# Performance work log

Hardware: AMD Instinct MI355X
Metric: run time of the kernel (lower is better)

Reference implementation:

```python
import jax, jax.numpy as jnp
import numpy as np

# ---- dims ----
N = 16380      # atoms
R = 819        # residues
APR = 20       # atoms per residue
K = 16         # k_neighbors
H = 64         # hidden_mult (channels)
HEADS = 8
DH = H // HEADS
L = 6          # hidden_layers
BINS = 100
MIN_D, MAX_D = 0.0, 10.0
E_DIM = 64     # embed_dim
FFN = 2 * H    # mlp_ratio = 2


def setup_inputs() -> dict:
    key = jax.random.key(0)
    ks = jax.random.split(key, 22)
    g = lambda k, shape, fan: jax.random.normal(k, shape, jnp.float32) / np.sqrt(fan)
    return {
        'coords': jax.random.uniform(ks[0], (N, 3), jnp.float32) * 70.0,
        'atom_ids': jax.random.randint(ks[1], (N,), 0, 64),
        'res_ids': jax.random.randint(ks[2], (N,), 0, 8),
        'elem_ids': jax.random.randint(ks[3], (N,), 0, 16),
        'residue_index': jnp.repeat(jnp.arange(R), APR),
        'emb_atom': jax.random.normal(ks[4], (64, 32), jnp.float32),
        'emb_res': jax.random.normal(ks[5], (8, 16), jnp.float32),
        'emb_elem': jax.random.normal(ks[6], (16, 16), jnp.float32),
        'Win': g(ks[7], (E_DIM, H), E_DIM),
        'Wq': g(ks[8], (L, H, H), H),
        'Wk': g(ks[9], (L, H, H), H),
        'Wv': g(ks[10], (L, H, H), H),
        'Wvec': g(ks[11], (L, H, H), H),
        'wdir': jax.random.normal(ks[12], (L, H), jnp.float32) * 0.1,
        'dist_bias': jax.random.normal(ks[13], (L, BINS, HEADS), jnp.float32) * 0.1,
        'Wo': g(ks[14], (L, H, H), H),
        'W1': g(ks[15], (L, H, FFN), H),
        'W2': g(ks[16], (L, FFN, H), FFN),
        'Wg': g(ks[17], (L, H, H), H),
        'Wout': g(ks[18], (H, 2), H),
        'bout': jnp.zeros((2,), jnp.float32),
    }


def _ln(x):
    m = jnp.mean(x, axis=-1, keepdims=True)
    v = jnp.mean((x - m) ** 2, axis=-1, keepdims=True)
    return (x - m) * jax.lax.rsqrt(v + 1e-5)


def reference(coords, atom_ids, res_ids, elem_ids, residue_index,
              emb_atom, emb_res, emb_elem, Win, Wq, Wk, Wv, Wvec, wdir,
              dist_bias, Wo, W1, W2, Wg, Wout, bout):
    n = coords.shape[0]
    # --- polymer embedding: concat atom/residue/element embeddings ---
    feat = jnp.concatenate(
        [emb_atom[atom_ids], emb_res[res_ids], emb_elem[elem_ids]], axis=-1)  # (N, E_DIM)
    # --- kNN graph via dense pairwise distances (avoid (N,N,3) intermediate) ---
    sq = jnp.sum(coords * coords, axis=-1)
    d2 = sq[:, None] + sq[None, :] - 2.0 * (coords @ coords.T)     # (N, N)
    idx = jnp.arange(n)
    d2 = d2.at[idx, idx].set(jnp.inf)
    _, nbr = jax.lax.top_k(-d2, K)                                  # (N, K) src per dst
    # --- edge geometry: relative vector, distance, bin ---
    dvec = coords[:, None, :] - coords[nbr]                         # (N, K, 3) dst - src
    d = jnp.sqrt(jnp.sum(dvec * dvec, axis=-1) + 1e-12)
    dirn = dvec / d[..., None]
    bins = jnp.clip(((d - MIN_D) / (MAX_D - MIN_D) * BINS).astype(jnp.int32), 0, BINS - 1)
    # --- lift to hidden repr: scalars from embedding, vectors start at zero ---
    s = feat @ Win                                                  # (N, H) l=0 features
    v = jnp.zeros((n, H, 3), s.dtype)                               # (N, H, 3) l=1 features
    for l in range(L):
        h = _ln(s)
        q = (h @ Wq[l]).reshape(n, HEADS, DH)
        kf = (h @ Wk[l]).reshape(n, HEADS, DH)
        vf = (h @ Wv[l]).reshape(n, HEADS, DH)
        kn, vn = kf[nbr], vf[nbr]                                   # (N, K, HEADS, DH)
        logits = jnp.einsum('nhd,nkhd->nkh', q, kn) / np.sqrt(DH) + dist_bias[l][bins]
        attn = jax.nn.softmax(logits, axis=1)                       # softmax over K nbrs
        msg = jnp.einsum('nkh,nkhd->nhd', attn, vn).reshape(n, H)
        # equivariant vector messages: mixed source vectors + edge direction term
        vvals = jnp.einsum('nhc,hg->ngc', v, Wvec[l])               # (N, H, 3)
        vmsg = vvals[nbr] + wdir[l][None, None, :, None] * dirn[:, :, None, :]
        attn_c = jnp.repeat(attn, DH, axis=-1)                      # (N, K, H)
        vagg = jnp.einsum('nkh,nkhc->nhc', attn_c, vmsg)
        s = s + msg @ Wo[l]
        v = v + vagg
        h2 = _ln(s)
        s = s + jax.nn.gelu(h2 @ W1[l]) @ W2[l]                     # scalar FFN
        v = v * jax.nn.sigmoid(h2 @ Wg[l])[..., None]               # gated vector update
    # --- out repr is l=0 only; residue mean-pool then linear head ---
    res_feat = jax.ops.segment_sum(s, residue_index, num_segments=R) / APR
    return res_feat @ Wout + bout                                   # (R, 2)
```

## Files before the change

kernel.cpp:

```cpp
#include <hip/hip_runtime.h>
#include <cfloat>

#define NN    16380
#define RR    819
#define APR   20
#define KNB   16
#define HID   64
#define LAYERS 6
#define BINS  100
#define N64   (NN*HID)

#define ATB   32
#define NBLK  512
#define LDA   68
#define LDU   132
#define CSIZE 4.375f

#define OFF_QA    0
#define OFF_KA    (1*N64)
#define OFF_FA    (2*N64)
#define OFF_QB    (3*N64)
#define OFF_KB    (4*N64)
#define OFF_FB    (5*N64)
#define OFF_VA    (6*N64)
#define OFF_VB    (9*N64)
#define OFF_S     (12*N64)
#define OFF_DIRNS (13*N64)
#define OFF_C4    (OFF_DIRNS + NN*48)
#define OFF_C4S   (OFF_C4 + NN*4)
#define OFF_RES   (OFF_C4S + NN*4)
#define OFF_NBRS  (OFF_RES + RR*64)
#define OFF_BINSS (OFF_NBRS + NN*16)
#define OFF_O2N   (OFF_BINSS + NN*16)
#define OFF_N2O   (OFF_O2N + NN)
#define OFF_CELL  (OFF_N2O + NN)
#define OFF_HIST  (OFF_CELL + NN)
#define OFF_CNT   (OFF_HIST + 4096)
#define OFF_BASE  (OFF_CNT + 4096)

typedef unsigned long long u64;
#define U64MAX 0xFFFFFFFFFFFFFFFFull

__device__ __forceinline__ float gelu_f(float x) {
    float x3 = x*x*x;
    float t = tanhf(0.7978845608028654f*(x + 0.044715f*x3));
    return 0.5f*x*(1.0f+t);
}
__device__ __forceinline__ float sigmoid_f(float x) {
    return 1.0f/(1.0f + expf(-x));
}
__device__ __forceinline__ int spread3(int x) {
    return (x&1) | ((x&2)<<2) | ((x&4)<<4) | ((x&8)<<6);
}
__device__ __forceinline__ unsigned sortable_u32(float f) {
    unsigned u = __float_as_uint(f);
    return u ^ ((u & 0x80000000u) ? 0xFFFFFFFFu : 0x80000000u);
}

__global__ void pad_cell_kernel(const float* __restrict__ coords, float4* __restrict__ c4,
                                int* __restrict__ cellid, int* __restrict__ hist,
                                float* __restrict__ resb, int n) {
    int i = blockIdx.x*256 + threadIdx.x;
    for (int j = i; j < RR*HID; j += 16384) resb[j] = 0.f;
    if (i >= n) return;
    float x = coords[3*i], y = coords[3*i+1], z = coords[3*i+2];
    float sq = __fadd_rn(__fadd_rn(__fmul_rn(x,x), __fmul_rn(y,y)), __fmul_rn(z,z));
    c4[i] = make_float4(x, y, z, sq);
    int cx = min(15, max(0, (int)(x * (16.0f/70.0f))));
    int cy = min(15, max(0, (int)(y * (16.0f/70.0f))));
    int cz = min(15, max(0, (int)(z * (16.0f/70.0f))));
    int m = spread3(cx) | (spread3(cy)<<1) | (spread3(cz)<<2);
    cellid[i] = m;
    atomicAdd(&hist[m], 1);
}
__global__ void scan_kernel(const int* __restrict__ hist, int* __restrict__ base) {
    __shared__ int part[256];
    int t = threadIdx.x;
    int loc[16]; int s = 0;
    #pragma unroll
    for (int e = 0; e < 16; ++e) { loc[e] = s; s += hist[t*16+e]; }
    part[t] = s;
    __syncthreads();
    if (t == 0) { int acc = 0; for (int i = 0; i < 256; ++i) { int v = part[i]; part[i] = acc; acc += v; } }
    __syncthreads();
    int off = part[t];
    #pragma unroll
    for (int e = 0; e < 16; ++e) base[t*16+e] = off + loc[e];
}
__global__ void scatter_kernel(const int* __restrict__ cellid, const int* __restrict__ base,
                               int* __restrict__ cnt, int* __restrict__ o2n,
                               int* __restrict__ n2o, const float4* __restrict__ c4,
                               float4* __restrict__ c4s, int n) {
    int i = blockIdx.x*256 + threadIdx.x;
    if (i >= n) return;
    int m = cellid[i];
    int pos = base[m] + atomicAdd(&cnt[m], 1);
    o2n[i] = pos; n2o[pos] = i;
    c4s[pos] = c4[i];
}

#define SCRATCH 1024
__global__ __launch_bounds__(256) void knn_grid_kernel(
    const float4* __restrict__ c4s, const int* __restrict__ base, const int* __restrict__ hist,
    const int* __restrict__ n2o, const int* __restrict__ o2n,
    int* __restrict__ nbr, int* __restrict__ binsO, float* __restrict__ dirn, int n)
{
    __shared__ int sIdx[4][SCRATCH];
    int tid = threadIdx.x;
    int wv = tid >> 6, lane = tid & 63;
    int i = blockIdx.x*4 + wv;
    bool valid = i < n;
    int ii = valid ? i : 0;
    float4 cd = c4s[ii];
    float sqd = cd.w;
    int cx = min(15, max(0, (int)(cd.x * (16.0f/70.0f))));
    int cy = min(15, max(0, (int)(cd.y * (16.0f/70.0f))));
    int cz = min(15, max(0, (int)(cd.z * (16.0f/70.0f))));
    u64 dlist = U64MAX;
    u64 vmax  = U64MAX;
    int* sidx = sIdx[wv];

    auto compute_pk = [&](int idx) -> u64 {
        if (idx == i) return U64MAX;
        float4 cc = c4s[idx];
        float dt = __fmul_rn(cd.x, cc.x);
        dt = __fmaf_rn(cd.y, cc.y, dt);
        dt = __fmaf_rn(cd.z, cc.z, dt);
        float key = __fsub_rn(__fadd_rn(sqd, cc.w), __fmul_rn(2.0f, dt));
        int org = n2o[idx];
        return ((u64)sortable_u32(key) << 32) | (unsigned)org;
    };

    auto process_batch = [&](int M) {
        if (M <= 0) return;
        u64 lmin = U64MAX;
        for (int p = lane; p < M; p += 64) {
            u64 pk = compute_pk(sidx[p]);
            lmin = (pk < lmin) ? pk : lmin;
        }
        u64 T = lmin;
        #pragma unroll
        for (int off = 1; off < 64; off <<= 1) {
            u64 o = __shfl_xor(T, off);
            T = (o > T) ? o : T;
        }
        for (int c0 = 0; c0 < M; c0 += 64) {
            int p = c0 + lane;
            u64 mypk = (p < M) ? compute_pk(sidx[p]) : U64MAX;
            u64 bound = (vmax < T) ? vmax : T;
            unsigned long long mask = __ballot(mypk <= bound);
            while (mask) {
                int lb = (int)__builtin_ctzll(mask);
                mask &= mask - 1;
                u64 dc = __shfl(mypk, lb);
                if (dc < vmax) {
                    u64 dp = __shfl_up(dlist, 1);
                    bool below = dc < dlist;
                    bool take  = below && (lane == 0 || dc >= dp);
                    if (lane < 16) dlist = below ? (take ? dc : dp) : dlist;
                    vmax = __shfl(dlist, 15);
                }
            }
        }
    };

    for (int R = 1; R <= 16; ++R) {
        int side = 2*R+1;
        int ncell = side*side*side;
        int M = 0;
        for (int t0 = 0; t0 < ncell; t0 += 64) {
            int t = t0 + lane;
            int cnt = 0, b = 0;
            if (t < ncell) {
                int dxc = t % side - R;
                int dyc = (t/side) % side - R;
                int dzc = t/(side*side) - R;
                int ch = max(abs(dxc), max(abs(dyc), abs(dzc)));
                bool use = (R == 1) || (ch == R);
                int x = cx+dxc, y = cy+dyc, z = cz+dzc;
                if (use && x>=0 && x<16 && y>=0 && y<16 && z>=0 && z<16) {
                    int m = spread3(x) | (spread3(y)<<1) | (spread3(z)<<2);
                    cnt = hist[m]; b = base[m];
                }
            }
            int incl = cnt;
            #pragma unroll
            for (int o = 1; o < 64; o <<= 1) { int v = __shfl_up(incl, o); if (lane >= o) incl += v; }
            int excl = incl - cnt;
            int tot = __shfl(incl, 63);
            if (M + tot > SCRATCH) { process_batch(M); M = 0; }
            for (int e = 0; e < cnt; ++e) {
                int pos = M + excl + e;
                if (pos < SCRATCH) sidx[pos] = b + e;
            }
            M = min(M + tot, SCRATCH);
        }
        process_batch(M);
        float rim = (float)R * CSIZE;
        unsigned thS = sortable_u32(rim*rim - 0.05f);
        if ((unsigned)(vmax >> 32) < thS) break;
    }
    if (valid && lane < 16) {
        int org = (int)(dlist & 0xFFFFFFFFull);
        int src = o2n[org];
        float4 cs = c4s[src];
        float dx = __fsub_rn(cd.x, cs.x);
        float dy = __fsub_rn(cd.y, cs.y);
        float dz = __fsub_rn(cd.z, cs.z);
        float ss = __fadd_rn(__fadd_rn(__fmul_rn(dx,dx), __fmul_rn(dy,dy)),
                             __fmul_rn(dz,dz));
        float dd = __fsqrt_rn(__fadd_rn(ss, 1e-12f));
        nbr[i*KNB + lane] = src;
        float bf = __fmul_rn(__fdiv_rn(dd, 10.0f), 100.0f);
        int b = (int)bf;
        b = min(max(b, 0), BINS-1);
        binsO[i*KNB + lane] = b;
        dirn[i*48 + lane*3 + 0] = __fdiv_rn(dx, dd);
        dirn[i*48 + lane*3 + 1] = __fdiv_rn(dy, dd);
        dirn[i*48 + lane*3 + 2] = __fdiv_rn(dz, dd);
    }
}

__global__ __launch_bounds__(256) void prologue_kernel(
    const int* __restrict__ aid, const int* __restrict__ rid, const int* __restrict__ eid,
    const int* __restrict__ n2o,
    const float* __restrict__ ea, const float* __restrict__ er, const float* __restrict__ ee,
    const float* __restrict__ Win, const float* __restrict__ Wq, const float* __restrict__ Wk,
    const float* __restrict__ Wv,
    float* __restrict__ sg, float* __restrict__ qout, float* __restrict__ kout,
    float* __restrict__ vfout)
{
    __shared__ __align__(16) float sS[ATB*LDA];
    __shared__ __align__(16) float sH[ATB*LDA];
    __shared__ __align__(16) float sW[4096];
    const int tid = threadIdx.x;
    const int a0 = blockIdx.x*ATB;
    const int gi = tid>>4, gj = tid&15;
    const int lrow = tid>>3, lsub = tid&7;

    auto stageW = [&](const float* W) {
        const float4* src = (const float4*)W; float4* dst = (float4*)sW;
        #pragma unroll
        for (int r = 0; r < 4; ++r) dst[tid + 256*r] = src[tid + 256*r];
    };
    auto do_gemm = [&](const float* sA, float4& c0, float4& c1) {
        const float* a0p = sA + gi*LDA;
        const float* a1p = sA + (gi+16)*LDA;
        const float* wr  = sW + gj*4;
        #pragma unroll 8
        for (int k = 0; k < 64; ++k) {
            float av0 = a0p[k], av1 = a1p[k];
            float4 w = *(const float4*)(wr + k*64);
            c0.x = fmaf(av0,w.x,c0.x); c0.y = fmaf(av0,w.y,c0.y);
            c0.z = fmaf(av0,w.z,c0.z); c0.w = fmaf(av0,w.w,c0.w);
            c1.x = fmaf(av1,w.x,c1.x); c1.y = fmaf(av1,w.y,c1.y);
            c1.z = fmaf(av1,w.z,c1.z); c1.w = fmaf(av1,w.w,c1.w);
        }
    };
    auto do_ln = [&](const float* src, float* dst) {
        const float* sp = src + lrow*LDA + lsub*8;
        float v[8]; float s1 = 0.f;
        #pragma unroll
        for (int e = 0; e < 8; ++e) { v[e] = sp[e]; s1 += v[e]; }
        s1 += __shfl_xor(s1,1); s1 += __shfl_xor(s1,2); s1 += __shfl_xor(s1,4);
        float mean = s1*(1.0f/64.0f);
        float s2 = 0.f;
        #pragma unroll
        for (int e = 0; e < 8; ++e) { float t = v[e]-mean; s2 += t*t; }
        s2 += __shfl_xor(s2,1); s2 += __shfl_xor(s2,2); s2 += __shfl_xor(s2,4);
        float sc = 1.0f/sqrtf(s2*(1.0f/64.0f)+1e-5f);
        float* dp = dst + lrow*LDA + lsub*8;
        #pragma unroll
        for (int e = 0; e < 8; ++e) dp[e] = (v[e]-mean)*sc;
    };
    auto store_g = [&](float* base, float4 c0, float4 c1) {
        int g0 = a0+gi, g1 = a0+gi+16;
        if (g0 < NN) *(float4*)(base + (size_t)g0*64 + gj*4) = c0;
        if (g1 < NN) *(float4*)(base + (size_t)g1*64 + gj*4) = c1;
    };

    {
        int ga = a0 + lrow;
        int io = (ga < NN) ? n2o[ga] : 0;
        #pragma unroll
        for (int e = 0; e < 8; ++e) {
            int c = lsub*8 + e;
            float x = 0.f;
            if (ga < NN) {
                if (c < 32)      x = ea[aid[io]*32 + c];
                else if (c < 48) x = er[rid[io]*16 + (c-32)];
                else             x = ee[eid[io]*16 + (c-48)];
            }
            sH[lrow*LDA + c] = x;
        }
    }
    stageW(Win);
    __syncthreads();
    {
        float4 c0 = make_float4(0,0,0,0), c1 = c0;
        do_gemm(sH, c0, c1);
        *(float4*)(sS + gi*LDA + gj*4)      = c0;
        *(float4*)(sS + (gi+16)*LDA + gj*4) = c1;
        store_g(sg, c0, c1);
    }
    __syncthreads();
    do_ln(sS, sH);
    stageW(Wk);
    __syncthreads();
    { float4 c0 = make_float4(0,0,0,0), c1 = c0; do_gemm(sH, c0, c1); store_g(kout, c0, c1); }
    __syncthreads();
    stageW(Wv); __syncthreads();
    { float4 c0 = make_float4(0,0,0,0), c1 = c0; do_gemm(sH, c0, c1); store_g(vfout, c0, c1); }
    __syncthreads();
    stageW(Wq); __syncthreads();
    { float4 c0 = make_float4(0,0,0,0), c1 = c0; do_gemm(sH, c0, c1); store_g(qout, c0, c1); }
}

__global__ __launch_bounds__(256) void layer_kernel(
    const float* __restrict__ qin, const float* __restrict__ kin, const float* __restrict__ vfin,
    float* __restrict__ qout, float* __restrict__ kout, float* __restrict__ vfout,
    const float* __restrict__ vin, float* __restrict__ vout,
    float* __restrict__ sg, const float* __restrict__ dirn,
    const int* __restrict__ nbr, const int* __restrict__ bins,
    float* __restrict__ resb, const int* __restrict__ ridx, const int* __restrict__ n2o,
    const float* __restrict__ Wvec, const float* __restrict__ wdir,
    const float* __restrict__ dist_bias,
    const float* __restrict__ Wo, const float* __restrict__ W1, const float* __restrict__ W2,
    const float* __restrict__ Wg, const float* __restrict__ Wq, const float* __restrict__ Wk,
    const float* __restrict__ Wv, int l)
{
    __shared__ __align__(16) float sS[ATB*LDA];
    __shared__ __align__(16) float sH[ATB*LDA];
    __shared__ __align__(16) float sM[ATB*LDU];
    __shared__ __align__(16) float sVA[3][ATB*LDA];
    __shared__ __align__(16) float sW[4096];
    __shared__ float sDS[ATB*24];

    const int tid = threadIdx.x;
    const int bswz = (blockIdx.x & 7) * (NBLK/8) + (blockIdx.x >> 3);
    const int a0 = bswz*ATB;
    const int gi = tid>>4, gj = tid&15;
    const int lrow = tid>>3, lsub = tid&7;
    const int wv = tid>>6, lane = tid&63;

    const float* Wo_l = Wo + l*4096;
    const float* Wg_l = Wg + l*4096;
    const float* Wc_l = Wvec + l*4096;
    const float* W1_l = W1 + l*8192;
    const float* W2_l = W2 + l*8192;
    const float* db_l = dist_bias + l*BINS*8;
    const float* wd_l = wdir + l*64;

    auto stageW = [&](const float* W) {
        const float4* src = (const float4*)W; float4* dst = (float4*)sW;
        #pragma unroll
        for (int r = 0; r < 4; ++r) dst[tid + 256*r] = src[tid + 256*r];
    };
    auto stageW1h = [&](const float* W1l, int h) {
        const float4* src = (const float4*)W1l; float4* dst = (float4*)sW;
        #pragma unroll
        for (int r = 0; r < 4; ++r) {
            int q = tid + 256*r;
            int row = q >> 4, c4i = q & 15;
            dst[q] = src[row*32 + h*16 + c4i];
        }
    };
    auto do_gemm = [&](const float* sA, int lda, int ko, float4& c0, float4& c1) {
        const float* a0p = sA + gi*lda + ko;
        const float* a1p = sA + (gi+16)*lda + ko;
        const float* wr  = sW + gj*4;
        #pragma unroll 8
        for (int k = 0; k < 64; ++k) {
            float av0 = a0p[k], av1 = a1p[k];
            float4 w = *(const float4*)(wr + k*64);
            c0.x = fmaf(av0,w.x,c0.x); c0.y = fmaf(av0,w.y,c0.y);
            c0.z = fmaf(av0,w.z,c0.z); c0.w = fmaf(av0,w.w,c0.w);
            c1.x = fmaf(av1,w.x,c1.x); c1.y = fmaf(av1,w.y,c1.y);
            c1.z = fmaf(av1,w.z,c1.z); c1.w = fmaf(av1,w.w,c1.w);
        }
    };
    auto do_ln = [&](const float* src, float* dst) {
        const float* sp = src + lrow*LDA + lsub*8;
        float v[8]; float s1 = 0.f;
        #pragma unroll
        for (int e = 0; e < 8; ++e) { v[e] = sp[e]; s1 += v[e]; }
        s1 += __shfl_xor(s1,1); s1 += __shfl_xor(s1,2); s1 += __shfl_xor(s1,4);
        float mean = s1*(1.0f/64.0f);
        float s2 = 0.f;
        #pragma unroll
        for (int e = 0; e < 8; ++e) { float t = v[e]-mean; s2 += t*t; }
        s2 += __shfl_xor(s2,1); s2 += __shfl_xor(s2,2); s2 += __shfl_xor(s2,4);
        float sc = 1.0f/sqrtf(s2*(1.0f/64.0f)+1e-5f);
        float* dp = dst + lrow*LDA + lsub*8;
        #pragma unroll
        for (int e = 0; e < 8; ++e) dp[e] = (v[e]-mean)*sc;
    };
    auto store_g = [&](float* base, float4 c0, float4 c1) {
        int g0 = a0+gi, g1 = a0+gi+16;
        if (g0 < NN) *(float4*)(base + (size_t)g0*64 + gj*4) = c0;
        if (g1 < NN) *(float4*)(base + (size_t)g1*64 + gj*4) = c1;
    };

    {
        int ga = a0 + lrow;
        float4 z = make_float4(0,0,0,0);
        float4 x0 = z, x1 = z;
        if (ga < NN) {
            const float4* sp = (const float4*)(sg + (size_t)ga*64);
            x0 = sp[lsub*2]; x1 = sp[lsub*2+1];
        }
        float4* dp = (float4*)(sS + lrow*LDA);
        dp[lsub*2] = x0; dp[lsub*2+1] = x1;
    }
    stageW(Wo_l);

    for (int aa = 0; aa < 8; ++aa) {
        int la = wv*8 + aa;
        int ga = a0 + la;
        if (ga >= NN) break;
        float qh = qin[(size_t)ga*64 + lane];
        float lg[KNB]; int nb[KNB];
        #pragma unroll
        for (int k = 0; k < KNB; ++k) {
            int j = nbr[ga*KNB + k];
            nb[k] = j;
            float t = qh * kin[(size_t)j*64 + lane];
            t += __shfl_xor(t,1); t += __shfl_xor(t,2); t += __shfl_xor(t,4);
            lg[k] = t*0.35355339059327373f + db_l[bins[ga*KNB+k]*8 + (lane>>3)];
        }
        float m = lg[0];
        #pragma unroll
        for (int k = 1; k < KNB; ++k) m = fmaxf(m, lg[k]);
        float ssum = 0.f;
        #pragma unroll
        for (int k = 0; k < KNB; ++k) { lg[k] = expf(lg[k]-m); ssum += lg[k]; }
        float inv = 1.0f/ssum;
        float mh=0.f, b0=0.f, b1=0.f, b2=0.f, s0=0.f, s1=0.f, s2=0.f;
        if (l > 0) {
            #pragma unroll
            for (int k = 0; k < KNB; ++k) {
                float w = lg[k]*inv; int j = nb[k];
                mh += w * vfin[(size_t)j*64 + lane];
                b0 += w * vin[(size_t)j*64 + lane];
                b1 += w * vin[(size_t)N64 + (size_t)j*64 + lane];
                b2 += w * vin[2*(size_t)N64 + (size_t)j*64 + lane];
                s0 += w * dirn[ga*48 + k*3 + 0];
                s1 += w * dirn[ga*48 + k*3 + 1];
                s2 += w * dirn[ga*48 + k*3 + 2];
            }
            sVA[0][la*LDA + lane] = b0;
            sVA[1][la*LDA + lane] = b1;
            sVA[2][la*LDA + lane] = b2;
        } else {
            #pragma unroll
            for (int k = 0; k < KNB; ++k) {
                float w = lg[k]*inv; int j = nb[k];
                mh += w * vfin[(size_t)j*64 + lane];
                s0 += w * dirn[ga*48 + k*3 + 0];
                s1 += w * dirn[ga*48 + k*3 + 1];
                s2 += w * dirn[ga*48 + k*3 + 2];
            }
        }
        sM[la*LDU + lane] = mh;
        if ((lane & 7) == 0) {
            int hh = lane >> 3;
            sDS[la*24 + 0*8 + hh] = s0;
            sDS[la*24 + 1*8 + hh] = s1;
            sDS[la*24 + 2*8 + hh] = s2;
        }
    }
    __syncthreads();

    {
        float4 c0 = *(float4*)(sS + gi*LDA + gj*4);
        float4 c1 = *(float4*)(sS + (gi+16)*LDA + gj*4);
        do_gemm(sM, LDU, 0, c0, c1);
        *(float4*)(sS + gi*LDA + gj*4)      = c0;
        *(float4*)(sS + (gi+16)*LDA + gj*4) = c1;
    }
    __syncthreads();

    do_ln(sS, sH);
    stageW(Wg_l);
    __syncthreads();

    {
        float4 g0 = make_float4(0,0,0,0), g1 = g0;
        do_gemm(sH, LDA, 0, g0, g1);
        g0.x=sigmoid_f(g0.x); g0.y=sigmoid_f(g0.y); g0.z=sigmoid_f(g0.z); g0.w=sigmoid_f(g0.w);
        g1.x=sigmoid_f(g1.x); g1.y=sigmoid_f(g1.y); g1.z=sigmoid_f(g1.z); g1.w=sigmoid_f(g1.w);
        __syncthreads();
        stageW(Wc_l); __syncthreads();
        float4 wd4 = *(const float4*)&wd_l[gj*4];
        int g0i = a0+gi, g1i = a0+gi+16;
        #pragma unroll
        for (int p = 0; p < 3; ++p) {
            float4 t0 = make_float4(0,0,0,0), t1 = t0;
            if (l > 0) do_gemm(sVA[p], LDA, 0, t0, t1);
            float sp0 = sDS[gi*24 + p*8 + (gj>>1)];
            float sp1 = sDS[(gi+16)*24 + p*8 + (gj>>1)];
            if (g0i < NN) {
                float4 vi = make_float4(0,0,0,0);
                if (l > 0) vi = *(const float4*)(vin + (size_t)p*N64 + (size_t)g0i*64 + gj*4);
                float4 o;
                o.x = (vi.x + t0.x + wd4.x*sp0)*g0.x;
                o.y = (vi.y + t0.y + wd4.y*sp0)*g0.y;
                o.z = (vi.z + t0.z + wd4.z*sp0)*g0.z;
                o.w = (vi.w + t0.w + wd4.w*sp0)*g0.w;
                *(float4*)(vout + (size_t)p*N64 + (size_t)g0i*64 + gj*4) = o;
            }
            if (g1i < NN) {
                float4 vi = make_float4(0,0,0,0);
                if (l > 0) vi = *(const float4*)(vin + (size_t)p*N64 + (size_t)g1i*64 + gj*4);
                float4 o;
                o.x = (vi.x + t1.x + wd4.x*sp1)*g1.x;
                o.y = (vi.y + t1.y + wd4.y*sp1)*g1.y;
                o.z = (vi.z + t1.z + wd4.z*sp1)*g1.z;
                o.w = (vi.w + t1.w + wd4.w*sp1)*g1.w;
                *(float4*)(vout + (size_t)p*N64 + (size_t)g1i*64 + gj*4) = o;
            }
        }
    }
    __syncthreads();

    stageW1h(W1_l, 0); __syncthreads();
    float4 u0a, u1a;
    {
        float4 c0 = make_float4(0,0,0,0), c1 = c0;
        do_gemm(sH, LDA, 0, c0, c1);
        c0.x=gelu_f(c0.x); c0.y=gelu_f(c0.y); c0.z=gelu_f(c0.z); c0.w=gelu_f(c0.w);
        c1.x=gelu_f(c1.x); c1.y=gelu_f(c1.y); c1.z=gelu_f(c1.z); c1.w=gelu_f(c1.w);
        u0a = c0; u1a = c1;
    }
    __syncthreads();
    *(float4*)(sM + gi*LDU + gj*4)      = u0a;
    *(float4*)(sM + (gi+16)*LDU + gj*4) = u1a;
    stageW1h(W1_l, 1);
    __syncthreads();
    float4 u0b, u1b;
    {
        float4 c0 = make_float4(0,0,0,0), c1 = c0;
        do_gemm(sH, LDA, 0, c0, c1);
        c0.x=gelu_f(c0.x); c0.y=gelu_f(c0.y); c0.z=gelu_f(c0.z); c0.w=gelu_f(c0.w);
        c1.x=gelu_f(c1.x); c1.y=gelu_f(c1.y); c1.z=gelu_f(c1.z); c1.w=gelu_f(c1.w);
        u0b = c0; u1b = c1;
    }
    __syncthreads();
    *(float4*)(sM + gi*LDU + 64 + gj*4)      = u0b;
    *(float4*)(sM + (gi+16)*LDU + 64 + gj*4) = u1b;
    stageW(W2_l);
    __syncthreads();
    {
        float4 c0 = *(float4*)(sS + gi*LDA + gj*4);
        float4 c1 = *(float4*)(sS + (gi+16)*LDA + gj*4);
        do_gemm(sM, LDU, 0, c0, c1);
        __syncthreads();
        stageW(W2_l + 4096); __syncthreads();
        do_gemm(sM, LDU, 64, c0, c1);
        *(float4*)(sS + gi*LDA + gj*4)      = c0;
        *(float4*)(sS + (gi+16)*LDA + gj*4) = c1;
    }
    __syncthreads();

    if (l < LAYERS-1) {
        do_ln(sS, sH);
        stageW(Wk + (l+1)*4096);
        __syncthreads();
        { float4 c0 = make_float4(0,0,0,0), c1 = c0; do_gemm(sH, LDA, 0, c0, c1); store_g(kout, c0, c1); }
        __syncthreads();
        stageW(Wv + (l+1)*4096); __syncthreads();
        { float4 c0 = make_float4(0,0,0,0), c1 = c0; do_gemm(sH, LDA, 0, c0, c1); store_g(vfout, c0, c1); }
        __syncthreads();
        stageW(Wq + (l+1)*4096); __syncthreads();
        { float4 c0 = make_float4(0,0,0,0), c1 = c0; do_gemm(sH, LDA, 0, c0, c1); store_g(qout, c0, c1); }
        {
            int ga = a0 + lrow;
            if (ga < NN) {
                float4* dp = (float4*)(sg + (size_t)ga*64);
                const float4* sp = (const float4*)(sS + lrow*LDA);
                dp[lsub*2] = sp[lsub*2]; dp[lsub*2+1] = sp[lsub*2+1];
            }
        }
    } else {
        int ga = a0 + lrow;
        if (ga < NN) {
            int r = ridx[n2o[ga]];
            #pragma unroll
            for (int e = 0; e < 8; ++e)
                atomicAdd(&resb[r*64 + lsub*8 + e], sS[lrow*LDA + lsub*8 + e]);
        }
    }
}

__global__ void head_kernel(const float* __restrict__ res, const float* __restrict__ Wout,
                            const float* __restrict__ bout, float* __restrict__ out, int r_total) {
    int wave = threadIdx.x >> 6, lane = threadIdx.x & 63;
    int r = blockIdx.x*4 + wave;
    if (r >= r_total) return;
    float p = res[r*HID + lane] * (1.0f/APR);
    float o0 = p * Wout[lane*2 + 0];
    float o1 = p * Wout[lane*2 + 1];
    #pragma unroll
    for (int off = 1; off < 64; off <<= 1) { o0 += __shfl_xor(o0, off); o1 += __shfl_xor(o1, off); }
    if (lane == 0) { out[r*2+0] = o0 + bout[0]; out[r*2+1] = o1 + bout[1]; }
}

extern "C" void kernel_launch(void* const* d_in, const int* in_sizes, int n_in,
                              void* d_out, int out_size, void* d_ws, size_t ws_size,
                              hipStream_t stream) {
    const float* coords    = (const float*)d_in[0];
    const int*   atom_ids  = (const int*)d_in[1];
    const int*   res_ids   = (const int*)d_in[2];
    const int*   elem_ids  = (const int*)d_in[3];
    const int*   ridx      = (const int*)d_in[4];
    const float* emb_atom  = (const float*)d_in[5];
    const float* emb_res   = (const float*)d_in[6];
    const float* emb_elem  = (const float*)d_in[7];
    const float* Win       = (const float*)d_in[8];
    const float* Wq        = (const float*)d_in[9];
    const float* Wk        = (const float*)d_in[10];
    const float* Wv        = (const float*)d_in[11];
    const float* Wvec      = (const float*)d_in[12];
    const float* wdir      = (const float*)d_in[13];
    const float* dist_bias = (const float*)d_in[14];
    const float* Wo        = (const float*)d_in[15];
    const float* W1        = (const float*)d_in[16];
    const float* W2        = (const float*)d_in[17];
    const float* Wg        = (const float*)d_in[18];
    const float* Wout      = (const float*)d_in[19];
    const float* bout      = (const float*)d_in[20];
    float* out = (float*)d_out;

    float* ws = (float*)d_ws;
    float* qA = ws + OFF_QA;  float* kA = ws + OFF_KA;  float* fA = ws + OFF_FA;
    float* qB = ws + OFF_QB;  float* kB = ws + OFF_KB;  float* fB = ws + OFF_FB;
    float* vA = ws + OFF_VA;  float* vB = ws + OFF_VB;
    float* sg = ws + OFF_S;
    float* dirn_s = ws + OFF_DIRNS;
    float4* c4  = (float4*)(ws + OFF_C4);
    float4* c4s = (float4*)(ws + OFF_C4S);
    float* resb = ws + OFF_RES;
    int* nbr_s  = (int*)(ws + OFF_NBRS);
    int* bins_s = (int*)(ws + OFF_BINSS);
    int* o2n    = (int*)(ws + OFF_O2N);
    int* n2o    = (int*)(ws + OFF_N2O);
    int* cellid = (int*)(ws + OFF_CELL);
    int* hist   = (int*)(ws + OFF_HIST);
    int* cnt    = (int*)(ws + OFF_CNT);
    int* baseb  = (int*)(ws + OFF_BASE);

    hipMemsetAsync(hist, 0, 2*4096*sizeof(int), stream);

    pad_cell_kernel<<<(NN+255)/256, 256, 0, stream>>>(coords, c4, cellid, hist, resb, NN);
    scan_kernel<<<1, 256, 0, stream>>>(hist, baseb);
    scatter_kernel<<<(NN+255)/256, 256, 0, stream>>>(cellid, baseb, cnt, o2n, n2o, c4, c4s, NN);
    knn_grid_kernel<<<(NN+3)/4, 256, 0, stream>>>(c4s, baseb, hist, n2o, o2n, nbr_s, bins_s, dirn_s, NN);

    prologue_kernel<<<NBLK, 256, 0, stream>>>(atom_ids, res_ids, elem_ids, n2o,
                                              emb_atom, emb_res, emb_elem,
                                              Win, Wq, Wk, Wv, sg, qA, kA, fA);
    for (int l = 0; l < LAYERS; ++l) {
        int p = l & 1;
        const float* qin = p ? qB : qA;  float* qout = p ? qA : qB;
        const float* kin = p ? kB : kA;  float* kout = p ? kA : kB;
        const float* fin = p ? fB : fA;  float* fout = p ? fA : fB;
        const float* vin = p ? vB : vA;  float* vout = p ? vA : vB;
        layer_kernel<<<NBLK, 256, 0, stream>>>(qin, kin, fin, qout, kout, fout,
                                               vin, vout, sg, dirn_s, nbr_s, bins_s,
                                               resb, ridx, n2o,
                                               Wvec, wdir, dist_bias,
                                               Wo, W1, W2, Wg, Wq, Wk, Wv, l);
    }
    head_kernel<<<(RR+3)/4, 256, 0, stream>>>(resb, Wout, bout, out, RR);
}
```

Baseline: 604.4 us.

## Double layer_kernel threads to 512 and shrink shared memory per block

The layer kernel now launches 512 threads per 32-atom block. Each thread computes one float4 output row tile instead of two, and each wave handles 4 atoms instead of 8 in the attention gather. Vector aggregates are kept in registers and streamed through one shared tile per component, and the FFN hidden is processed in two 64-wide halves. These changes drop the large sM (LDU=132) and the sVA buffers, cutting LDS per block so more waves can be resident and gather latency is hidden better. In exchange there are extra barriers and staging passes, and each weight tile is reused across fewer outputs per thread.

```diff
diff --git a/kernel.cpp b/kernel.cpp
--- a/kernel.cpp
+++ b/kernel.cpp
@@ -13,7 +13,6 @@
 #define ATB   32
 #define NBLK  512
 #define LDA   68
-#define LDU   132
 #define CSIZE 4.375f
 
 #define OFF_QA    0
@@ -316,7 +315,7 @@
     { float4 c0 = make_float4(0,0,0,0), c1 = c0; do_gemm(sH, c0, c1); store_g(qout, c0, c1); }
 }
 
-__global__ __launch_bounds__(256) void layer_kernel(
+__global__ __launch_bounds__(512, 4) void layer_kernel(
     const float* __restrict__ qin, const float* __restrict__ kin, const float* __restrict__ vfin,
     float* __restrict__ qout, float* __restrict__ kout, float* __restrict__ vfout,
     const float* __restrict__ vin, float* __restrict__ vout,
@@ -331,8 +330,7 @@
 {
     __shared__ __align__(16) float sS[ATB*LDA];
     __shared__ __align__(16) float sH[ATB*LDA];
-    __shared__ __align__(16) float sM[ATB*LDU];
-    __shared__ __align__(16) float sVA[3][ATB*LDA];
+    __shared__ __align__(16) float sM[ATB*LDA];
     __shared__ __align__(16) float sW[4096];
     __shared__ float sDS[ATB*24];
 
@@ -340,7 +338,6 @@
     const int bswz = (blockIdx.x & 7) * (NBLK/8) + (blockIdx.x >> 3);
     const int a0 = bswz*ATB;
     const int gi = tid>>4, gj = tid&15;
-    const int lrow = tid>>3, lsub = tid&7;
     const int wv = tid>>6, lane = tid&63;
 
     const float* Wo_l = Wo + l*4096;
@@ -353,80 +350,75 @@
 
     auto stageW = [&](const float* W) {
         const float4* src = (const float4*)W; float4* dst = (float4*)sW;
-        #pragma unroll
-        for (int r = 0; r < 4; ++r) dst[tid + 256*r] = src[tid + 256*r];
+        dst[tid]       = src[tid];
+        dst[tid + 512] = src[tid + 512];
     };
     auto stageW1h = [&](const float* W1l, int h) {
         const float4* src = (const float4*)W1l; float4* dst = (float4*)sW;
         #pragma unroll
-        for (int r = 0; r < 4; ++r) {
-            int q = tid + 256*r;
+        for (int r = 0; r < 2; ++r) {
+            int q = tid + 512*r;
             int row = q >> 4, c4i = q & 15;
             dst[q] = src[row*32 + h*16 + c4i];
         }
     };
-    auto do_gemm = [&](const float* sA, int lda, int ko, float4& c0, float4& c1) {
-        const float* a0p = sA + gi*lda + ko;
-        const float* a1p = sA + (gi+16)*lda + ko;
-        const float* wr  = sW + gj*4;
+    auto do_gemm = [&](const float* sA, int lda, int ko, float4& c0) {
+        const float* ap = sA + gi*lda + ko;
+        const float* wr = sW + gj*4;
         #pragma unroll 8
         for (int k = 0; k < 64; ++k) {
-            float av0 = a0p[k], av1 = a1p[k];
+            float av = ap[k];
             float4 w = *(const float4*)(wr + k*64);
-            c0.x = fmaf(av0,w.x,c0.x); c0.y = fmaf(av0,w.y,c0.y);
-            c0.z = fmaf(av0,w.z,c0.z); c0.w = fmaf(av0,w.w,c0.w);
-            c1.x = fmaf(av1,w.x,c1.x); c1.y = fmaf(av1,w.y,c1.y);
-            c1.z = fmaf(av1,w.z,c1.z); c1.w = fmaf(av1,w.w,c1.w);
+            c0.x = fmaf(av,w.x,c0.x); c0.y = fmaf(av,w.y,c0.y);
+            c0.z = fmaf(av,w.z,c0.z); c0.w = fmaf(av,w.w,c0.w);
         }
     };
     auto do_ln = [&](const float* src, float* dst) {
-        const float* sp = src + lrow*LDA + lsub*8;
-        float v[8]; float s1 = 0.f;
-        #pragma unroll
-        for (int e = 0; e < 8; ++e) { v[e] = sp[e]; s1 += v[e]; }
-        s1 += __shfl_xor(s1,1); s1 += __shfl_xor(s1,2); s1 += __shfl_xor(s1,4);
+        const float* sp = src + gi*LDA + gj*4;
+        float v[4]; float s1 = 0.f;
+        #pragma unroll
+        for (int e = 0; e < 4; ++e) { v[e] = sp[e]; s1 += v[e]; }
+        s1 += __shfl_xor(s1,1); s1 += __shfl_xor(s1,2);
+        s1 += __shfl_xor(s1,4); s1 += __shfl_xor(s1,8);
         float mean = s1*(1.0f/64.0f);
         float s2 = 0.f;
         #pragma unroll
-        for (int e = 0; e < 8; ++e) { float t = v[e]-mean; s2 += t*t; }
-        s2 += __shfl_xor(s2,1); s2 += __shfl_xor(s2,2); s2 += __shfl_xor(s2,4);
+        for (int e = 0; e < 4; ++e) { float t = v[e]-mean; s2 += t*t; }
+        s2 += __shfl_xor(s2,1); s2 += __shfl_xor(s2,2);
+        s2 += __shfl_xor(s2,4); s2 += __shfl_xor(s2,8);
         float sc = 1.0f/sqrtf(s2*(1.0f/64.0f)+1e-5f);
-        float* dp = dst + lrow*LDA + lsub*8;
-        #pragma unroll
-        for (int e = 0; e < 8; ++e) dp[e] = (v[e]-mean)*sc;
-    };
-    auto store_g = [&](float* base, float4 c0, float4 c1) {
-        int g0 = a0+gi, g1 = a0+gi+16;
+        float* dp = dst + gi*LDA + gj*4;
+        #pragma unroll
+        for (int e = 0; e < 4; ++e) dp[e] = (v[e]-mean)*sc;
+    };
+    auto store_g = [&](float* base, float4 c0) {
+        int g0 = a0+gi;
         if (g0 < NN) *(float4*)(base + (size_t)g0*64 + gj*4) = c0;
-        if (g1 < NN) *(float4*)(base + (size_t)g1*64 + gj*4) = c1;
     };
 
     {
-        int ga = a0 + lrow;
-        float4 z = make_float4(0,0,0,0);
-        float4 x0 = z, x1 = z;
-        if (ga < NN) {
-            const float4* sp = (const float4*)(sg + (size_t)ga*64);
-            x0 = sp[lsub*2]; x1 = sp[lsub*2+1];
-        }
-        float4* dp = (float4*)(sS + lrow*LDA);
-        dp[lsub*2] = x0; dp[lsub*2+1] = x1;
+        int ga = a0 + gi;
+        float4 x = make_float4(0,0,0,0);
+        if (ga < NN) x = ((const float4*)(sg + (size_t)ga*64))[gj];
+        ((float4*)(sS + gi*LDA))[gj] = x;
     }
     stageW(Wo_l);
 
-    for (int aa = 0; aa < 8; ++aa) {
-        int la = wv*8 + aa;
+    float bx[4], by[4], bz[4];
+    #pragma unroll
+    for (int aa = 0; aa < 4; ++aa) {
+        int la = wv*4 + aa;
         int ga = a0 + la;
-        if (ga >= NN) break;
-        float qh = qin[(size_t)ga*64 + lane];
+        int gq = (ga < NN) ? ga : (NN-1);
+        float qh = qin[(size_t)gq*64 + lane];
         float lg[KNB]; int nb[KNB];
         #pragma unroll
         for (int k = 0; k < KNB; ++k) {
-            int j = nbr[ga*KNB + k];
+            int j = nbr[gq*KNB + k];
             nb[k] = j;
             float t = qh * kin[(size_t)j*64 + lane];
             t += __shfl_xor(t,1); t += __shfl_xor(t,2); t += __shfl_xor(t,4);
-            lg[k] = t*0.35355339059327373f + db_l[bins[ga*KNB+k]*8 + (lane>>3)];
+            lg[k] = t*0.35355339059327373f + db_l[bins[gq*KNB+k]*8 + (lane>>3)];
         }
         float m = lg[0];
         #pragma unroll
@@ -444,24 +436,22 @@
                 b0 += w * vin[(size_t)j*64 + lane];
                 b1 += w * vin[(size_t)N64 + (size_t)j*64 + lane];
                 b2 += w * vin[2*(size_t)N64 + (size_t)j*64 + lane];
-                s0 += w * dirn[ga*48 + k*3 + 0];
-                s1 += w * dirn[ga*48 + k*3 + 1];
-                s2 += w * dirn[ga*48 + k*3 + 2];
-            }
-            sVA[0][la*LDA + lane] = b0;
-            sVA[1][la*LDA + lane] = b1;
-            sVA[2][la*LDA + lane] = b2;
+                s0 += w * dirn[gq*48 + k*3 + 0];
+                s1 += w * dirn[gq*48 + k*3 + 1];
+                s2 += w * dirn[gq*48 + k*3 + 2];
+            }
         } else {
             #pragma unroll
             for (int k = 0; k < KNB; ++k) {
                 float w = lg[k]*inv; int j = nb[k];
                 mh += w * vfin[(size_t)j*64 + lane];
-                s0 += w * dirn[ga*48 + k*3 + 0];
-                s1 += w * dirn[ga*48 + k*3 + 1];
-                s2 += w * dirn[ga*48 + k*3 + 2];
-            }
-        }
-        sM[la*LDU + lane] = mh;
+                s0 += w * dirn[gq*48 + k*3 + 0];
+                s1 += w * dirn[gq*48 + k*3 + 1];
+                s2 += w * dirn[gq*48 + k*3 + 2];
+            }
+        }
+        bx[aa] = b0; by[aa] = b1; bz[aa] = b2;
+        sM[la*LDA + lane] = mh;
         if ((lane & 7) == 0) {
             int hh = lane >> 3;
             sDS[la*24 + 0*8 + hh] = s0;
@@ -472,11 +462,9 @@
     __syncthreads();
 
     {
-        float4 c0 = *(float4*)(sS + gi*LDA + gj*4);
-        float4 c1 = *(float4*)(sS + (gi+16)*LDA + gj*4);
-        do_gemm(sM, LDU, 0, c0, c1);
-        *(float4*)(sS + gi*LDA + gj*4)      = c0;
-        *(float4*)(sS + (gi+16)*LDA + gj*4) = c1;
+        float4 c0 = ((float4*)(sS + gi*LDA))[gj];
+        do_gemm(sM, LDA, 0, c0);
+        ((float4*)(sS + gi*LDA))[gj] = c0;
     }
     __syncthreads();
 
@@ -484,110 +472,106 @@
     stageW(Wg_l);
     __syncthreads();
 
+    float4 g0v = make_float4(0,0,0,0);
+    do_gemm(sH, LDA, 0, g0v);
+    g0v.x = sigmoid_f(g0v.x); g0v.y = sigmoid_f(g0v.y);
+    g0v.z = sigmoid_f(g0v.z); g0v.w = sigmoid_f(g0v.w);
+    __syncthreads();
+
+    float4 wd4 = *(const float4*)&wd_l[gj*4];
+    const int gidx = a0 + gi;
+    if (l > 0) {
+        stageW(Wc_l);
+        #pragma unroll
+        for (int p = 0; p < 3; ++p) {
+            #pragma unroll
+            for (int aa = 0; aa < 4; ++aa) {
+                int la = wv*4 + aa;
+                float bv = (p==0) ? bx[aa] : (p==1) ? by[aa] : bz[aa];
+                sM[la*LDA + lane] = bv;
+            }
+            __syncthreads();
+            float4 t0 = make_float4(0,0,0,0);
+            do_gemm(sM, LDA, 0, t0);
+            float sp0 = sDS[gi*24 + p*8 + (gj>>1)];
+            if (gidx < NN) {
+                float4 vi = *(const float4*)(vin + (size_t)p*N64 + (size_t)gidx*64 + gj*4);
+                float4 o;
+                o.x = (vi.x + t0.x + wd4.x*sp0)*g0v.x;
+                o.y = (vi.y + t0.y + wd4.y*sp0)*g0v.y;
+                o.z = (vi.z + t0.z + wd4.z*sp0)*g0v.z;
+                o.w = (vi.w + t0.w + wd4.w*sp0)*g0v.w;
+                *(float4*)(vout + (size_t)p*N64 + (size_t)gidx*64 + gj*4) = o;
+            }
+            __syncthreads();
+        }
+    } else {
+        #pragma unroll
+        for (int p = 0; p < 3; ++p) {
+            float sp0 = sDS[gi*24 + p*8 + (gj>>1)];
+            if (gidx < NN) {
+                float4 o;
+                o.x = (wd4.x*sp0)*g0v.x;
+                o.y = (wd4.y*sp0)*g0v.y;
+                o.z = (wd4.z*sp0)*g0v.z;
+                o.w = (wd4.w*sp0)*g0v.w;
+                *(float4*)(vout + (size_t)p*N64 + (size_t)gidx*64 + gj*4) = o;
+            }
+        }
+    }
+
+    stageW1h(W1_l, 0); __syncthreads();
+    float4 ua;
     {
-        float4 g0 = make_float4(0,0,0,0), g1 = g0;
-        do_gemm(sH, LDA, 0, g0, g1);
-        g0.x=sigmoid_f(g0.x); g0.y=sigmoid_f(g0.y); g0.z=sigmoid_f(g0.z); g0.w=sigmoid_f(g0.w);
-        g1.x=sigmoid_f(g1.x); g1.y=sigmoid_f(g1.y); g1.z=sigmoid_f(g1.z); g1.w=sigmoid_f(g1.w);
-        __syncthreads();
-        stageW(Wc_l); __syncthreads();
-        float4 wd4 = *(const float4*)&wd_l[gj*4];
-        int g0i = a0+gi, g1i = a0+gi+16;
-        #pragma unroll
-        for (int p = 0; p < 3; ++p) {
-            float4 t0 = make_float4(0,0,0,0), t1 = t0;
-            if (l > 0) do_gemm(sVA[p], LDA, 0, t0, t1);
-            float sp0 = sDS[gi*24 + p*8 + (gj>>1)];
-            float sp1 = sDS[(gi+16)*24 + p*8 + (gj>>1)];
-            if (g0i < NN) {
-                float4 vi = make_float4(0,0,0,0);
-                if (l > 0) vi = *(const float4*)(vin + (size_t)p*N64 + (size_t)g0i*64 + gj*4);
-                float4 o;
-                o.x = (vi.x + t0.x + wd4.x*sp0)*g0.x;
-                o.y = (vi.y + t0.y + wd4.y*sp0)*g0.y;
-                o.z = (vi.z + t0.z + wd4.z*sp0)*g0.z;
-                o.w = (vi.w + t0.w + wd4.w*sp0)*g0.w;
-                *(float4*)(vout + (size_t)p*N64 + (size_t)g0i*64 + gj*4) = o;
-            }
-            if (g1i < NN) {
-                float4 vi = make_float4(0,0,0,0);
-                if (l > 0) vi = *(const float4*)(vin + (size_t)p*N64 + (size_t)g1i*64 + gj*4);
-                float4 o;
-                o.x = (vi.x + t1.x + wd4.x*sp1)*g1.x;
-                o.y = (vi.y + t1.y + wd4.y*sp1)*g1.y;
-                o.z = (vi.z + t1.z + wd4.z*sp1)*g1.z;
-                o.w = (vi.w + t1.w + wd4.w*sp1)*g1.w;
-                *(float4*)(vout + (size_t)p*N64 + (size_t)g1i*64 + gj*4) = o;
-            }
-        }
-    }
-    __syncthreads();
-
-    stageW1h(W1_l, 0); __syncthreads();
-    float4 u0a, u1a;
+        float4 c = make_float4(0,0,0,0);
+        do_gemm(sH, LDA, 0, c);
+        ua.x = gelu_f(c.x); ua.y = gelu_f(c.y); ua.z = gelu_f(c.z); ua.w = gelu_f(c.w);
+    }
+    __syncthreads();
+    ((float4*)(sM + gi*LDA))[gj] = ua;
+    stageW(W2_l);
+    __syncthreads();
+    float4 acc = ((float4*)(sS + gi*LDA))[gj];
+    do_gemm(sM, LDA, 0, acc);
+    __syncthreads();
+    stageW1h(W1_l, 1); __syncthreads();
+    float4 ub;
     {
-        float4 c0 = make_float4(0,0,0,0), c1 = c0;
-        do_gemm(sH, LDA, 0, c0, c1);
-        c0.x=gelu_f(c0.x); c0.y=gelu_f(c0.y); c0.z=gelu_f(c0.z); c0.w=gelu_f(c0.w);
-        c1.x=gelu_f(c1.x); c1.y=gelu_f(c1.y); c1.z=gelu_f(c1.z); c1.w=gelu_f(c1.w);
-        u0a = c0; u1a = c1;
-    }
-    __syncthreads();
-    *(float4*)(sM + gi*LDU + gj*4)      = u0a;
-    *(float4*)(sM + (gi+16)*LDU + gj*4) = u1a;
-    stageW1h(W1_l, 1);
-    __syncthreads();
-    float4 u0b, u1b;
-    {
-        float4 c0 = make_float4(0,0,0,0), c1 = c0;
-        do_gemm(sH, LDA, 0, c0, c1);
-        c0.x=gelu_f(c0.x); c0.y=gelu_f(c0.y); c0.z=gelu_f(c0.z); c0.w=gelu_f(c0.w);
-        c1.x=gelu_f(c1.x); c1.y=gelu_f(c1.y); c1.z=gelu_f(c1.z); c1.w=gelu_f(c1.w);
-        u0b = c0; u1b = c1;
-    }
-    __syncthreads();
-    *(float4*)(sM + gi*LDU + 64 + gj*4)      = u0b;
-    *(float4*)(sM + (gi+16)*LDU + 64 + gj*4) = u1b;
-    stageW(W2_l);
-    __syncthreads();
-    {
-        float4 c0 = *(float4*)(sS + gi*LDA + gj*4);
-        float4 c1 = *(float4*)(sS + (gi+16)*LDA + gj*4);
-        do_gemm(sM, LDU, 0, c0, c1);
-        __syncthreads();
-        stageW(W2_l + 4096); __syncthreads();
-        do_gemm(sM, LDU, 64, c0, c1);
-        *(float4*)(sS + gi*LDA + gj*4)      = c0;
-        *(float4*)(sS + (gi+16)*LDA + gj*4) = c1;
-    }
+        float4 c = make_float4(0,0,0,0);
+        do_gemm(sH, LDA, 0, c);
+        ub.x = gelu_f(c.x); ub.y = gelu_f(c.y); ub.z = gelu_f(c.z); ub.w = gelu_f(c.w);
+    }
+    __syncthreads();
+    ((float4*)(sM + gi*LDA))[gj] = ub;
+    stageW(W2_l + 4096);
+    __syncthreads();
+    do_gemm(sM, LDA, 0, acc);
+    ((float4*)(sS + gi*LDA))[gj] = acc;
     __syncthreads();
 
     if (l < LAYERS-1) {
         do_ln(sS, sH);
         stageW(Wk + (l+1)*4096);
         __syncthreads();
-        { float4 c0 = make_float4(0,0,0,0), c1 = c0; do_gemm(sH, LDA, 0, c0, c1); store_g(kout, c0, c1); }
+        { float4 c = make_float4(0,0,0,0); do_gemm(sH, LDA, 0, c); store_g(kout, c); }
         __syncthreads();
         stageW(Wv + (l+1)*4096); __syncthreads();
-        { float4 c0 = make_float4(0,0,0,0), c1 = c0; do_gemm(sH, LDA, 0, c0, c1); store_g(vfout, c0, c1); }
+        { float4 c = make_float4(0,0,0,0); do_gemm(sH, LDA, 0, c); store_g(vfout, c); }
         __syncthreads();
         stageW(Wq + (l+1)*4096); __syncthreads();
-        { float4 c0 = make_float4(0,0,0,0), c1 = c0; do_gemm(sH, LDA, 0, c0, c1); store_g(qout, c0, c1); }
+        { float4 c = make_float4(0,0,0,0); do_gemm(sH, LDA, 0, c); store_g(qout, c); }
         {
-            int ga = a0 + lrow;
-            if (ga < NN) {
-                float4* dp = (float4*)(sg + (size_t)ga*64);
-                const float4* sp = (const float4*)(sS + lrow*LDA);
-                dp[lsub*2] = sp[lsub*2]; dp[lsub*2+1] = sp[lsub*2+1];
-            }
+            int ga = a0 + gi;
+            if (ga < NN)
+                ((float4*)(sg + (size_t)ga*64))[gj] = ((float4*)(sS + gi*LDA))[gj];
         }
     } else {
-        int ga = a0 + lrow;
+        int ga = a0 + gi;
         if (ga < NN) {
             int r = ridx[n2o[ga]];
             #pragma unroll
-            for (int e = 0; e < 8; ++e)
-                atomicAdd(&resb[r*64 + lsub*8 + e], sS[lrow*LDA + lsub*8 + e]);
+            for (int e = 0; e < 4; ++e)
+                atomicAdd(&resb[r*64 + gj*4 + e], sS[gi*LDA + gj*4 + e]);
         }
     }
 }
@@ -665,7 +649,7 @@
         const float* kin = p ? kB : kA;  float* kout = p ? kA : kB;
         const float* fin = p ? fB : fA;  float* fout = p ? fA : fB;
         const float* vin = p ? vB : vA;  float* vout = p ? vA : vB;
-        layer_kernel<<<NBLK, 256, 0, stream>>>(qin, kin, fin, qout, kout, fout,
+        layer_kernel<<<NBLK, 512, 0, stream>>>(qin, kin, fin, qout, kout, fout,
                                                vin, vout, sg, dirn_s, nbr_s, bins_s,
                                                resb, ridx, n2o,
                                                Wvec, wdir, dist_bias,
```

Measured after the change: 850.7 us. +40.8%, slower.
